# Optimization experiments

Measured on AMD Instinct MI355X. Metric: run time of the kernel, lower is better.

## Reference

```python
import jax, jax.numpy as jnp
import numpy as np

DIM = 768
HEADS = 12
HEAD_DIM = DIM // HEADS  # 64
GRID = 48               # H = W = 48 tokens
RANK = 8                # LoRA rank


def setup_inputs() -> dict:
    key = jax.random.key(0)
    ks = jax.random.split(key, 20)
    s = 0.02
    inp = {
        "x": jax.random.normal(ks[0], (1, GRID, GRID, DIM), dtype=jnp.float32),
        "Wq": jax.random.normal(ks[1], (DIM, DIM), dtype=jnp.float32) * s,
        "bq": jax.random.normal(ks[2], (DIM,), dtype=jnp.float32) * s,
        "Wk": jax.random.normal(ks[3], (DIM, DIM), dtype=jnp.float32) * s,
        "bk": jax.random.normal(ks[4], (DIM,), dtype=jnp.float32) * s,
        "Wv": jax.random.normal(ks[5], (DIM, DIM), dtype=jnp.float32) * s,
        "bv": jax.random.normal(ks[6], (DIM,), dtype=jnp.float32) * s,
        "Wp": jax.random.normal(ks[7], (DIM, DIM), dtype=jnp.float32) * s,
        "bp": jax.random.normal(ks[8], (DIM,), dtype=jnp.float32) * s,
        "rel_pos_h": jax.random.normal(ks[9], (2 * GRID - 1, HEAD_DIM), dtype=jnp.float32) * s,
        "rel_pos_w": jax.random.normal(ks[10], (2 * GRID - 1, HEAD_DIM), dtype=jnp.float32) * s,
        "Aq": jax.random.normal(ks[11], (DIM, RANK), dtype=jnp.float32) * s,
        "Bq": jax.random.normal(ks[12], (RANK, DIM), dtype=jnp.float32) * s,
        "Ak": jax.random.normal(ks[13], (DIM, RANK), dtype=jnp.float32) * s,
        "Bk": jax.random.normal(ks[14], (RANK, DIM), dtype=jnp.float32) * s,
        "Av": jax.random.normal(ks[15], (DIM, RANK), dtype=jnp.float32) * s,
        "Bv": jax.random.normal(ks[16], (RANK, DIM), dtype=jnp.float32) * s,
    }
    return inp


def _get_rel_pos(size, rel_pos):
    # q_size == k_size == size, rel_pos has exactly 2*size-1 rows -> direct lookup
    idx = jnp.arange(size)[:, None] - jnp.arange(size)[None, :] + (size - 1)
    return rel_pos[idx]  # (size, size, head_dim)


def reference(x, Wq, bq, Wk, bk, Wv, bv, Wp, bp, rel_pos_h, rel_pos_w,
              Aq, Bq, Ak, Bk, Av, Bv):
    B, H, W, _ = x.shape
    N = H * W
    scale = HEAD_DIM ** -0.5

    # QKV projections + LoRA additions
    q = x @ Wq + bq + (x @ Aq) @ Bq
    k = x @ Wk + bk + (x @ Ak) @ Bk
    v = x @ Wv + bv + (x @ Av) @ Bv

    # (B, heads, N, head_dim)
    q = q.reshape(B, N, HEADS, HEAD_DIM).transpose(0, 2, 1, 3)
    k = k.reshape(B, N, HEADS, HEAD_DIM).transpose(0, 2, 1, 3)
    v = v.reshape(B, N, HEADS, HEAD_DIM).transpose(0, 2, 1, 3)

    attn = jnp.einsum('bhnc,bhmc->bhnm', q, k) * scale  # (B, heads, N, N)

    # Decomposed relative position bias (SAM add_decomposed_rel_pos)
    Rh = _get_rel_pos(H, rel_pos_h)  # (H, H, c)
    Rw = _get_rel_pos(W, rel_pos_w)  # (W, W, c)
    r_q = q.reshape(B, HEADS, H, W, HEAD_DIM)
    rel_h = jnp.einsum('bnhwc,hkc->bnhwk', r_q, Rh)  # (B, heads, H, W, H)
    rel_w = jnp.einsum('bnhwc,wkc->bnhwk', r_q, Rw)  # (B, heads, H, W, W)
    attn = (attn.reshape(B, HEADS, H, W, H, W)
            + rel_h[..., :, None] + rel_w[..., None, :]).reshape(B, HEADS, N, N)

    attn = jax.nn.softmax(attn, axis=-1)
    out = jnp.einsum('bhnm,bhmc->bhnc', attn, v)        # (B, heads, N, c)
    out = out.transpose(0, 2, 1, 3).reshape(B, H, W, DIM)
    return out @ Wp + bp
```

## Files before the change

kernel.cpp:

```cpp
#include <hip/hip_runtime.h>


#define DIM   768
#define HEADS 12
#define HD    64
#define NTOK  2304
#define RANK  8
#define GRD   48
#define CHUNKS 4
#define LOG2E 1.44269504088896f

typedef __attribute__((ext_vector_type(8))) short bf16x8;
typedef __attribute__((ext_vector_type(4))) float f32x4;
typedef unsigned short ushort_t;

__device__ __forceinline__ unsigned short f2bf(float x) {
    union { float f; unsigned u; } v; v.f = x;
    unsigned r = v.u + 0x7fffu + ((v.u >> 16) & 1u);
    return (unsigned short)(r >> 16);
}
__device__ __forceinline__ float bf2f(unsigned short h) {
    return __uint_as_float(((unsigned)h) << 16);
}

__device__ __forceinline__ void gload_lds16(const ushort_t* g, ushort_t* l) {
    __builtin_amdgcn_global_load_lds(
        (const __attribute__((address_space(1))) unsigned int*)g,
        (__attribute__((address_space(3))) unsigned int*)l, 16, 0, 0);
}

__global__ __launch_bounds__(256) void k_convert_x(
    const float* __restrict__ x, ushort_t* __restrict__ xb,
    const float* __restrict__ rph, const float* __restrict__ rpw,
    ushort_t* __restrict__ rphb, ushort_t* __restrict__ rpwb) {
    if (blockIdx.x < 1728) {
        int idx = (blockIdx.x * 256 + threadIdx.x) * 4;
        float4 v = *(const float4*)(x + idx);
        ushort4 o = make_ushort4(f2bf(v.x), f2bf(v.y), f2bf(v.z), f2bf(v.w));
        *(ushort4*)(xb + idx) = o;
    } else {
        int e = ((blockIdx.x - 1728) * 256 + threadIdx.x) * 4;
        const int TSZ = (2 * GRD - 1) * HD;
        if (e < TSZ) {
            float4 v = *(const float4*)(rph + e);
            ushort4 o = make_ushort4(f2bf(v.x), f2bf(v.y), f2bf(v.z), f2bf(v.w));
            *(ushort4*)(rphb + e) = o;
        } else if (e < 2 * TSZ) {
            float4 v = *(const float4*)(rpw + e - TSZ);
            ushort4 o = make_ushort4(f2bf(v.x), f2bf(v.y), f2bf(v.z), f2bf(v.w));
            *(ushort4*)(rpwb + e - TSZ) = o;
        }
    }
}

__global__ __launch_bounds__(256) void k_fold(
    const float* __restrict__ Wq, const float* __restrict__ Wk,
    const float* __restrict__ Wv, const float* __restrict__ Wp,
    const float* __restrict__ Aq, const float* __restrict__ Bq,
    const float* __restrict__ Ak, const float* __restrict__ Bk,
    const float* __restrict__ Av, const float* __restrict__ Bv,
    ushort_t* __restrict__ WT) {
    int kb = blockIdx.x * 32;
    int nb = blockIdx.y * 32;
    int qkv = nb / DIM;
    int nmod = nb % DIM;
    const float* W = (qkv == 0) ? Wq : (qkv == 1) ? Wk : (qkv == 2) ? Wv : Wp;
    const float* A = (qkv == 0) ? Aq : (qkv == 1) ? Ak : Av;
    const float* B = (qkv == 0) ? Bq : (qkv == 1) ? Bk : Bv;

    __shared__ float T[32][33];
    for (int i = threadIdx.x; i < 1024; i += 256) {
        int kl = i / 32, nl = i % 32;
        float v = W[(kb + kl) * DIM + nmod + nl];
        if (qkv < 3) {
            #pragma unroll
            for (int r = 0; r < RANK; r++)
                v += A[(kb + kl) * RANK + r] * B[r * DIM + nmod + nl];
        }
        T[kl][nl] = v;
    }
    __syncthreads();
    for (int i = threadIdx.x; i < 1024; i += 256) {
        int nl = i / 32, kl = i % 32;
        WT[(size_t)(nb + nl) * DIM + kb + kl] = f2bf(T[kl][nl]);
    }
}

__global__ __launch_bounds__(256) void k_gemm_qkv(
    const ushort_t* __restrict__ xb, const ushort_t* __restrict__ WT,
    const float* __restrict__ bq, const float* __restrict__ bk,
    const float* __restrict__ bv,
    ushort_t* __restrict__ Qb, ushort_t* __restrict__ Kb,
    ushort_t* __restrict__ Vtb) {
    __shared__ __align__(16) ushort_t As[128 * 32];
    __shared__ __align__(16) ushort_t Bs[128 * 32];
    int tid = threadIdx.x;
    int wave = tid >> 6, lane = tid & 63, quad = lane >> 4, l16 = lane & 15;
    int wx = wave & 1, wy = wave >> 1;
    int nb = blockIdx.x * 128, mb = blockIdx.y * 128;

    f32x4 zero = {0.f, 0.f, 0.f, 0.f};
    f32x4 acc[4][4];
    #pragma unroll
    for (int i = 0; i < 4; i++)
        #pragma unroll
        for (int j = 0; j < 4; j++) acc[i][j] = zero;

    int rl = lane >> 2;
    int cl = (lane & 3) * 8;
    const ushort_t* gA = xb + (size_t)(mb + wave * 32 + rl) * DIM + cl;
    const ushort_t* gB = WT + (size_t)(nb + wave * 32 + rl) * DIM + cl;
    ushort_t* lA = &As[(wave * 32) * 32];
    ushort_t* lB = &Bs[(wave * 32) * 32];

    for (int k0 = 0; k0 < DIM; k0 += 32) {
        __syncthreads();
        gload_lds16(gA + k0,            lA);
        gload_lds16(gA + k0 + 16 * DIM, lA + 16 * 32);
        gload_lds16(gB + k0,            lB);
        gload_lds16(gB + k0 + 16 * DIM, lB + 16 * 32);
        __syncthreads();
        bf16x8 af[4], bf[4];
        #pragma unroll
        for (int i = 0; i < 4; i++)
            af[i] = *(const bf16x8*)&As[(wy * 64 + i * 16 + l16) * 32 + quad * 8];
        #pragma unroll
        for (int j = 0; j < 4; j++)
            bf[j] = *(const bf16x8*)&Bs[(wx * 64 + j * 16 + l16) * 32 + quad * 8];
        #pragma unroll
        for (int i = 0; i < 4; i++)
            #pragma unroll
            for (int j = 0; j < 4; j++)
                acc[i][j] = __builtin_amdgcn_mfma_f32_16x16x32_bf16(af[i], bf[j], acc[i][j], 0, 0, 0);
    }

    #pragma unroll
    for (int j = 0; j < 4; j++) {
        int col = nb + wx * 64 + j * 16 + l16;
        int qkv = col / DIM, rem = col % DIM;
        int hh = rem >> 6, cc = rem & 63;
        const float* bias = (qkv == 0) ? bq : (qkv == 1) ? bk : bv;
        float bval = bias[rem];
        #pragma unroll
        for (int i = 0; i < 4; i++) {
            #pragma unroll
            for (int r = 0; r < 4; r++) {
                int row = mb + wy * 64 + i * 16 + quad * 4 + r;
                unsigned short o = f2bf(acc[i][j][r] + bval);
                if (qkv == 0)      Qb[(size_t)(hh * NTOK + row) * HD + cc] = o;
                else if (qkv == 1) Kb[(size_t)(hh * NTOK + row) * HD + cc] = o;
                else               Vtb[(size_t)(hh * HD + cc) * NTOK + row] = o;
            }
        }
    }
}

__global__ __launch_bounds__(256) void k_relmm(
    const ushort_t* __restrict__ Qb, const ushort_t* __restrict__ rphb,
    const ushort_t* __restrict__ rpwb, float* __restrict__ relH,
    float* __restrict__ relW) {
    int id = blockIdx.x * 4 + (threadIdx.x >> 6);
    int lane = threadIdx.x & 63, quad = lane >> 4, l16 = lane & 15;
    bool isW = id >= 576;
    int t = isW ? id - 576 : id;
    int h = t / GRD, g = t % GRD;
    const ushort_t* tab = isW ? rpwb : rphb;
    float* outp = isW ? relW : relH;

    f32x4 zero = {0.f, 0.f, 0.f, 0.f};
    f32x4 acc[3][3];
    #pragma unroll
    for (int i = 0; i < 3; i++)
        #pragma unroll
        for (int j = 0; j < 3; j++) acc[i][j] = zero;

    bf16x8 bfr[3][2];
    #pragma unroll
    for (int ct = 0; ct < 3; ct++) {
        int trow = g + 47 - (ct * 16 + l16);
        bfr[ct][0] = *(const bf16x8*)&tab[(size_t)trow * HD + quad * 8];
        bfr[ct][1] = *(const bf16x8*)&tab[(size_t)trow * HD + 32 + quad * 8];
    }
    #pragma unroll
    for (int ms = 0; ms < 3; ms++) {
        int m = ms * 16 + l16;
        int n = isW ? m * GRD + g : g * GRD + m;
        bf16x8 a0 = *(const bf16x8*)&Qb[(size_t)(h * NTOK + n) * HD + quad * 8];
        bf16x8 a1 = *(const bf16x8*)&Qb[(size_t)(h * NTOK + n) * HD + 32 + quad * 8];
        #pragma unroll
        for (int ct = 0; ct < 3; ct++) {
            acc[ms][ct] = __builtin_amdgcn_mfma_f32_16x16x32_bf16(a0, bfr[ct][0], acc[ms][ct], 0, 0, 0);
            acc[ms][ct] = __builtin_amdgcn_mfma_f32_16x16x32_bf16(a1, bfr[ct][1], acc[ms][ct], 0, 0, 0);
        }
    }
    #pragma unroll
    for (int ms = 0; ms < 3; ms++) {
        #pragma unroll
        for (int ct = 0; ct < 3; ct++) {
            #pragma unroll
            for (int r = 0; r < 4; r++) {
                int m = ms * 16 + quad * 4 + r;
                int n = isW ? m * GRD + g : g * GRD + m;
                int col = ct * 16 + l16;
                outp[(size_t)(h * NTOK + n) * GRD + col] = acc[ms][ct][r] * LOG2E;
            }
        }
    }
}

__global__ __launch_bounds__(256) void k_attn(
    const ushort_t* __restrict__ Qb, const ushort_t* __restrict__ Kb,
    const ushort_t* __restrict__ Vtb, const float* __restrict__ relH,
    const float* __restrict__ relW, float* __restrict__ Opart,
    float* __restrict__ Lpart) {
    int h = blockIdx.x >> 2, chunk = blockIdx.x & 3, qt = blockIdx.y;
    int tid = threadIdx.x;
    int wave = tid >> 6, lane = tid & 63, quad = lane >> 4, l16 = lane & 15;
    int qbase = qt * 128;
    int kbase = chunk * 576;

    __shared__ __align__(16) ushort_t Ks[64 * 68];
    __shared__ __align__(16) ushort_t Vs[64 * 68];
    __shared__ __align__(16) ushort_t Ps[4][32 * 68];
    __shared__ __align__(16) ushort_t rws[128 * 52];
    __shared__ __align__(16) ushort_t rhs[128 * 14];

    for (int i = tid; i < 128 * 48; i += 256) {
        int r = i / 48, c = i % 48;
        rws[r * 52 + c] = f2bf(relW[(size_t)(h * NTOK + qbase + r) * GRD + c]);
    }
    for (int i = tid; i < 128 * 12; i += 256) {
        int r = i / 12, c = i % 12;
        rhs[r * 14 + c] = f2bf(relH[(size_t)(h * NTOK + qbase + r) * GRD + chunk * 12 + c]);
    }

    bf16x8 qf[2][2];
    #pragma unroll
    for (int s = 0; s < 2; s++) {
        int qrow = qbase + wave * 32 + s * 16 + l16;
        qf[s][0] = *(const bf16x8*)&Qb[(size_t)(h * NTOK + qrow) * HD + quad * 8];
        qf[s][1] = *(const bf16x8*)&Qb[(size_t)(h * NTOK + qrow) * HD + 32 + quad * 8];
    }

    int r0 = tid >> 3, c0 = (tid & 7) * 8;
    const ushort_t* kg0 = Kb + (size_t)(h * NTOK + r0) * HD + c0;
    const ushort_t* kg1 = Kb + (size_t)(h * NTOK + r0 + 32) * HD + c0;
    const ushort_t* vg0 = Vtb + (size_t)(h * HD + r0) * NTOK + c0;
    const ushort_t* vg1 = Vtb + (size_t)(h * HD + r0 + 32) * NTOK + c0;
    int sk0 = r0 * 68 + c0, sk1 = sk0 + 32 * 68;

    float lacc[2] = {0.f, 0.f};
    f32x4 zero = {0.f, 0.f, 0.f, 0.f};
    f32x4 oacc[2][4];
    #pragma unroll
    for (int s = 0; s < 2; s++)
        #pragma unroll
        for (int cs = 0; cs < 4; cs++) oacc[s][cs] = zero;

    const float scale2 = 0.125f * LOG2E;

    uint4 rk0 = *(const uint4*)(kg0 + (size_t)kbase * HD);
    uint4 rk1 = *(const uint4*)(kg1 + (size_t)kbase * HD);
    uint4 rv0 = *(const uint4*)(vg0 + kbase);
    uint4 rv1 = *(const uint4*)(vg1 + kbase);

    for (int kt = 0; kt < 9; kt++) {
        int kb = kbase + kt * 64;
        __syncthreads();
        *(uint4*)&Ks[sk0] = rk0;  *(uint4*)&Ks[sk1] = rk1;
        *(uint4*)&Vs[sk0] = rv0;  *(uint4*)&Vs[sk1] = rv1;
        __syncthreads();
        if (kt < 8) {
            int kbn = kb + 64;
            rk0 = *(const uint4*)(kg0 + (size_t)kbn * HD);
            rk1 = *(const uint4*)(kg1 + (size_t)kbn * HD);
            rv0 = *(const uint4*)(vg0 + kbn);
            rv1 = *(const uint4*)(vg1 + kbn);
        }

        #pragma unroll
        for (int ks = 0; ks < 4; ks++) {
            bf16x8 kf0 = *(const bf16x8*)&Ks[(ks * 16 + l16) * 68 + quad * 8];
            bf16x8 kf1 = *(const bf16x8*)&Ks[(ks * 16 + l16) * 68 + 32 + quad * 8];
            f32x4 st[2];
            #pragma unroll
            for (int s = 0; s < 2; s++) {
                f32x4 z = zero;
                z = __builtin_amdgcn_mfma_f32_16x16x32_bf16(kf0, qf[s][0], z, 0, 0, 0);
                z = __builtin_amdgcn_mfma_f32_16x16x32_bf16(kf1, qf[s][1], z, 0, 0, 0);
                st[s] = z;
            }
            int kb4 = kb + ks * 16 + quad * 4;
            int kh = kb4 / 48;
            int khl = kh - chunk * 12;
            int kw0 = kb4 - kh * 48;
            #pragma unroll
            for (int s = 0; s < 2; s++) {
                int row = wave * 32 + s * 16 + l16;
                float rh = bf2f(rhs[row * 14 + khl]);
                uint2 u = *(const uint2*)&rws[row * 52 + kw0];
                float p0 = __builtin_amdgcn_exp2f(st[s][0] * scale2 + rh + __uint_as_float(u.x << 16));
                float p1 = __builtin_amdgcn_exp2f(st[s][1] * scale2 + rh + __uint_as_float(u.x & 0xffff0000u));
                float p2 = __builtin_amdgcn_exp2f(st[s][2] * scale2 + rh + __uint_as_float(u.y << 16));
                float p3 = __builtin_amdgcn_exp2f(st[s][3] * scale2 + rh + __uint_as_float(u.y & 0xffff0000u));
                lacc[s] += (p0 + p1) + (p2 + p3);
                uint2 w;
                w.x = __builtin_amdgcn_perm(__float_as_uint(p1), __float_as_uint(p0), 0x07060302u);
                w.y = __builtin_amdgcn_perm(__float_as_uint(p3), __float_as_uint(p2), 0x07060302u);
                *(uint2*)&Ps[wave][(s * 16 + l16) * 68 + ks * 16 + quad * 4] = w;
            }
        }

        bf16x8 vf[4][2];
        #pragma unroll
        for (int cs = 0; cs < 4; cs++) {
            vf[cs][0] = *(const bf16x8*)&Vs[(cs * 16 + l16) * 68 + quad * 8];
            vf[cs][1] = *(const bf16x8*)&Vs[(cs * 16 + l16) * 68 + 32 + quad * 8];
        }
        #pragma unroll
        for (int s = 0; s < 2; s++) {
            bf16x8 pa0 = *(const bf16x8*)&Ps[wave][(s * 16 + l16) * 68 + quad * 8];
            bf16x8 pa1 = *(const bf16x8*)&Ps[wave][(s * 16 + l16) * 68 + 32 + quad * 8];
            #pragma unroll
            for (int cs = 0; cs < 4; cs++) {
                oacc[s][cs] = __builtin_amdgcn_mfma_f32_16x16x32_bf16(pa0, vf[cs][0], oacc[s][cs], 0, 0, 0);
                oacc[s][cs] = __builtin_amdgcn_mfma_f32_16x16x32_bf16(pa1, vf[cs][1], oacc[s][cs], 0, 0, 0);
            }
        }
    }

    #pragma unroll
    for (int s = 0; s < 2; s++) {
        float l = lacc[s];
        l += __shfl_xor(l, 16);
        l += __shfl_xor(l, 32);
        lacc[s] = l;
    }

    size_t obase = (size_t)(chunk * HEADS + h) * NTOK;
    #pragma unroll
    for (int s = 0; s < 2; s++) {
        #pragma unroll
        for (int cs = 0; cs < 4; cs++) {
            #pragma unroll
            for (int r = 0; r < 4; r++) {
                int row = qbase + wave * 32 + s * 16 + quad * 4 + r;
                Opart[(obase + row) * HD + cs * 16 + l16] = oacc[s][cs][r];
            }
        }
        if (quad == 0)
            Lpart[obase + qbase + wave * 32 + s * 16 + l16] = lacc[s];
    }
}

__global__ __launch_bounds__(256) void k_merge(const float* __restrict__ Opart,
                                               const float* __restrict__ Lpart,
                                               ushort_t* __restrict__ Ob) {
    int t = blockIdx.x * 256 + threadIdx.x;
    int e = t * 4;
    int c = e & (HD - 1);
    int row = (e >> 6) % NTOK;
    int h = e / (NTOK * HD);
    const int ostride = HEADS * NTOK * HD;
    float4 s = {0.f, 0.f, 0.f, 0.f};
    float l = 0.f;
    #pragma unroll
    for (int ch = 0; ch < CHUNKS; ch++) {
        float4 v = *(const float4*)&Opart[(size_t)ch * ostride + e];
        s.x += v.x; s.y += v.y; s.z += v.z; s.w += v.w;
        l += Lpart[(size_t)(ch * HEADS + h) * NTOK + row];
    }
    float inv = 1.0f / l;
    ushort4 o = make_ushort4(f2bf(s.x * inv), f2bf(s.y * inv),
                             f2bf(s.z * inv), f2bf(s.w * inv));
    *(ushort4*)&Ob[(size_t)row * DIM + h * HD + c] = o;
}

__global__ __launch_bounds__(256) void k_gemm_proj(
    const ushort_t* __restrict__ Ob, const ushort_t* __restrict__ WTp,
    const float* __restrict__ bp, float* __restrict__ out) {
    __shared__ __align__(16) ushort_t As[128 * 40];
    __shared__ __align__(16) ushort_t Bs[128 * 40];
    int tid = threadIdx.x;
    int wave = tid >> 6, lane = tid & 63, quad = lane >> 4, l16 = lane & 15;
    int wx = wave & 1, wy = wave >> 1;
    int nb = blockIdx.x * 128, mb = blockIdx.y * 128;

    f32x4 zero = {0.f, 0.f, 0.f, 0.f};
    f32x4 acc[4][4];
    #pragma unroll
    for (int i = 0; i < 4; i++)
        #pragma unroll
        for (int j = 0; j < 4; j++) acc[i][j] = zero;

    const ushort_t* Ag = Ob + (size_t)(mb + (tid >> 1)) * DIM + (tid & 1) * 16;
    const ushort_t* Bg = WTp + (size_t)(nb + (tid >> 1)) * DIM + (tid & 1) * 16;
    int sidx = (tid >> 1) * 40 + (tid & 1) * 16;

    for (int k0 = 0; k0 < DIM; k0 += 32) {
        uint4 a0 = *(const uint4*)(Ag + k0);
        uint4 a1 = *(const uint4*)(Ag + k0 + 8);
        uint4 b0 = *(const uint4*)(Bg + k0);
        uint4 b1 = *(const uint4*)(Bg + k0 + 8);
        __syncthreads();
        *(uint4*)&As[sidx] = a0;  *(uint4*)&As[sidx + 8] = a1;
        *(uint4*)&Bs[sidx] = b0;  *(uint4*)&Bs[sidx + 8] = b1;
        __syncthreads();
        bf16x8 af[4], bf[4];
        #pragma unroll
        for (int i = 0; i < 4; i++)
            af[i] = *(const bf16x8*)&As[(wy * 64 + i * 16 + l16) * 40 + quad * 8];
        #pragma unroll
        for (int j = 0; j < 4; j++)
            bf[j] = *(const bf16x8*)&Bs[(wx * 64 + j * 16 + l16) * 40 + quad * 8];
        #pragma unroll
        for (int i = 0; i < 4; i++)
            #pragma unroll
            for (int j = 0; j < 4; j++)
                acc[i][j] = __builtin_amdgcn_mfma_f32_16x16x32_bf16(af[i], bf[j], acc[i][j], 0, 0, 0);
    }

    #pragma unroll
    for (int j = 0; j < 4; j++) {
        int col = nb + wx * 64 + j * 16 + l16;
        float bval = bp[col];
        #pragma unroll
        for (int i = 0; i < 4; i++) {
            #pragma unroll
            for (int r = 0; r < 4; r++) {
                int row = mb + wy * 64 + i * 16 + quad * 4 + r;
                out[(size_t)row * DIM + col] = acc[i][j][r] + bval;
            }
        }
    }
}

extern "C" void kernel_launch(void* const* d_in, const int* in_sizes, int n_in,
                              void* d_out, int out_size, void* d_ws, size_t ws_size,
                              hipStream_t stream) {
    const float* x   = (const float*)d_in[0];
    const float* Wq  = (const float*)d_in[1];
    const float* bq  = (const float*)d_in[2];
    const float* Wk  = (const float*)d_in[3];
    const float* bk  = (const float*)d_in[4];
    const float* Wv  = (const float*)d_in[5];
    const float* bv  = (const float*)d_in[6];
    const float* Wp  = (const float*)d_in[7];
    const float* bp  = (const float*)d_in[8];
    const float* rph = (const float*)d_in[9];
    const float* rpw = (const float*)d_in[10];
    const float* Aq  = (const float*)d_in[11];
    const float* Bq  = (const float*)d_in[12];
    const float* Ak  = (const float*)d_in[13];
    const float* Bk  = (const float*)d_in[14];
    const float* Av  = (const float*)d_in[15];
    const float* Bv  = (const float*)d_in[16];
    float* out = (float*)d_out;

    char* w = (char*)d_ws;
    size_t off = 0;
    auto carve = [&](size_t bytes) {
        char* p = w + off;
        off += (bytes + 255) & ~(size_t)255;
        return p;
    };
    ushort_t* xb    = (ushort_t*)carve((size_t)NTOK * DIM * 2);
    ushort_t* WT    = (ushort_t*)carve((size_t)4 * DIM * DIM * 2);
    ushort_t* Qb    = (ushort_t*)carve((size_t)HEADS * NTOK * HD * 2);
    ushort_t* Kb    = (ushort_t*)carve((size_t)HEADS * NTOK * HD * 2);
    ushort_t* Vtb   = (ushort_t*)carve((size_t)HEADS * HD * NTOK * 2);
    float*    relH  = (float*)carve((size_t)HEADS * NTOK * GRD * 4);
    float*    relW  = (float*)carve((size_t)HEADS * NTOK * GRD * 4);
    ushort_t* Ob    = (ushort_t*)carve((size_t)NTOK * DIM * 2);
    float*    Opart = (float*)carve((size_t)CHUNKS * HEADS * NTOK * HD * 4);
    float*    Lpart = (float*)carve((size_t)CHUNKS * HEADS * NTOK * 4);
    ushort_t* rphb  = (ushort_t*)carve((size_t)(2 * GRD - 1) * HD * 2);
    ushort_t* rpwb  = (ushort_t*)carve((size_t)(2 * GRD - 1) * HD * 2);

    k_convert_x<<<dim3(1728 + 12), dim3(256), 0, stream>>>(x, xb, rph, rpw, rphb, rpwb);
    k_fold<<<dim3(DIM / 32, 4 * DIM / 32), dim3(256), 0, stream>>>(
        Wq, Wk, Wv, Wp, Aq, Bq, Ak, Bk, Av, Bv, WT);
    k_gemm_qkv<<<dim3(18, 18), dim3(256), 0, stream>>>(
        xb, WT, bq, bk, bv, Qb, Kb, Vtb);
    k_relmm<<<dim3(288), dim3(256), 0, stream>>>(
        Qb, rphb, rpwb, relH, relW);
    k_attn<<<dim3(HEADS * CHUNKS, NTOK / 128), dim3(256), 0, stream>>>(
        Qb, Kb, Vtb, relH, relW, Opart, Lpart);
    k_merge<<<dim3(HEADS * NTOK * HD / (256 * 4)), dim3(256), 0, stream>>>(
        Opart, Lpart, Ob);
    k_gemm_proj<<<dim3(6, 18), dim3(256), 0, stream>>>(
        Ob, WT + (size_t)3 * DIM * DIM, bp, out);
}
```

Baseline: 213.6 us.

## Fuse all stages into one cooperative persistent kernel with grid syncs

Replaces the seven separate launches with a single cooperative kernel of 768 persistent blocks. Each former kernel becomes a phase, and the phases are separated by grid-wide barriers. The attention phase also keeps the relW bias in registers as packed bf16 instead of staging it in shared memory, which cuts LDS use so four blocks fit per CU. This is meant to remove launch overhead and inter-kernel gaps, at the cost of grid-sync latency and of leaving many blocks idle in phases with few tiles (for example 108 blocks in the projection GEMM). A fallback to the multi-kernel path is kept for devices without cooperative launch support.

```diff
diff --git a/kernel.cpp b/kernel.cpp
--- a/kernel.cpp
+++ b/kernel.cpp
@@ -1,4 +1,7 @@
 #include <hip/hip_runtime.h>
+#include <hip/hip_cooperative_groups.h>
+
+namespace cg = cooperative_groups;
 
 
 #define DIM   768
@@ -9,6 +12,7 @@
 #define GRD   48
 #define CHUNKS 4
 #define LOG2E 1.44269504088896f
+#define NBLK  768
 
 typedef __attribute__((ext_vector_type(8))) short bf16x8;
 typedef __attribute__((ext_vector_type(4))) float f32x4;
@@ -22,11 +26,410 @@
 __device__ __forceinline__ float bf2f(unsigned short h) {
     return __uint_as_float(((unsigned)h) << 16);
 }
-
 __device__ __forceinline__ void gload_lds16(const ushort_t* g, ushort_t* l) {
     __builtin_amdgcn_global_load_lds(
         (const __attribute__((address_space(1))) unsigned int*)g,
         (__attribute__((address_space(3))) unsigned int*)l, 16, 0, 0);
+}
+
+struct MonoP {
+    const float *x, *Wq, *bq, *Wk, *bk, *Wv, *bv, *Wp, *bp, *rph, *rpw,
+                *Aq, *Bq, *Ak, *Bk, *Av, *Bv;
+    float *out;
+    ushort_t *xb, *WT, *Qb, *Kb, *Vtb, *Ob, *rphb, *rpwb;
+    float *relH, *relW, *Opart, *Lpart;
+};
+
+__global__ __launch_bounds__(256, 4) void k_mono(MonoP P) {
+    cg::grid_group gg = cg::this_grid();
+    __shared__ __align__(16) unsigned char smem[38912];
+    const int bid = blockIdx.x, tid = threadIdx.x;
+    const int wave = tid >> 6, lane = tid & 63, quad = lane >> 4, l16 = lane & 15;
+    const f32x4 zero = {0.f, 0.f, 0.f, 0.f};
+
+    for (int ct = bid; ct < 1740; ct += NBLK) {
+        if (ct < 1728) {
+            int idx = (ct * 256 + tid) * 4;
+            float4 v = *(const float4*)(P.x + idx);
+            ushort4 o = make_ushort4(f2bf(v.x), f2bf(v.y), f2bf(v.z), f2bf(v.w));
+            *(ushort4*)(P.xb + idx) = o;
+        } else {
+            int e = ((ct - 1728) * 256 + tid) * 4;
+            const int TSZ = (2 * GRD - 1) * HD;
+            if (e < TSZ) {
+                float4 v = *(const float4*)(P.rph + e);
+                ushort4 o = make_ushort4(f2bf(v.x), f2bf(v.y), f2bf(v.z), f2bf(v.w));
+                *(ushort4*)(P.rphb + e) = o;
+            } else if (e < 2 * TSZ) {
+                float4 v = *(const float4*)(P.rpw + e - TSZ);
+                ushort4 o = make_ushort4(f2bf(v.x), f2bf(v.y), f2bf(v.z), f2bf(v.w));
+                *(ushort4*)(P.rpwb + e - TSZ) = o;
+            }
+        }
+    }
+    {
+        float* T = (float*)smem;
+        for (int ft = bid; ft < 2304; ft += NBLK) {
+            int kb = (ft % 24) * 32, nb = (ft / 24) * 32;
+            int sel = nb / DIM, nmod = nb % DIM;
+            const float* W = (sel == 0) ? P.Wq : (sel == 1) ? P.Wk : (sel == 2) ? P.Wv : P.Wp;
+            const float* A = (sel == 0) ? P.Aq : (sel == 1) ? P.Ak : P.Av;
+            const float* B = (sel == 0) ? P.Bq : (sel == 1) ? P.Bk : P.Bv;
+            for (int i = tid; i < 1024; i += 256) {
+                int kl = i >> 5, nl = i & 31;
+                float v = W[(kb + kl) * DIM + nmod + nl];
+                if (sel < 3) {
+                    #pragma unroll
+                    for (int r = 0; r < RANK; r++)
+                        v += A[(kb + kl) * RANK + r] * B[r * DIM + nmod + nl];
+                }
+                T[kl * 33 + nl] = v;
+            }
+            __syncthreads();
+            for (int i = tid; i < 1024; i += 256) {
+                int nl = i >> 5, kl = i & 31;
+                P.WT[(size_t)(nb + nl) * DIM + kb + kl] = f2bf(T[kl * 33 + nl]);
+            }
+            __syncthreads();
+        }
+    }
+    gg.sync();
+
+    if (bid < 324) {
+        ushort_t* As = (ushort_t*)smem;
+        ushort_t* Bs = (ushort_t*)(smem + 8192);
+        int wx = wave & 1, wy = wave >> 1;
+        int nb = (bid % 18) * 128, mb = (bid / 18) * 128;
+
+        f32x4 acc[4][4];
+        #pragma unroll
+        for (int i = 0; i < 4; i++)
+            #pragma unroll
+            for (int j = 0; j < 4; j++) acc[i][j] = zero;
+
+        int rl = lane >> 2, cl = (lane & 3) * 8;
+        const ushort_t* gA = P.xb + (size_t)(mb + wave * 32 + rl) * DIM + cl;
+        const ushort_t* gB = P.WT + (size_t)(nb + wave * 32 + rl) * DIM + cl;
+        ushort_t* lA = &As[(wave * 32) * 32];
+        ushort_t* lB = &Bs[(wave * 32) * 32];
+
+        for (int k0 = 0; k0 < DIM; k0 += 32) {
+            __syncthreads();
+            gload_lds16(gA + k0,            lA);
+            gload_lds16(gA + k0 + 16 * DIM, lA + 16 * 32);
+            gload_lds16(gB + k0,            lB);
+            gload_lds16(gB + k0 + 16 * DIM, lB + 16 * 32);
+            __syncthreads();
+            bf16x8 af[4], bf[4];
+            #pragma unroll
+            for (int i = 0; i < 4; i++)
+                af[i] = *(const bf16x8*)&As[(wy * 64 + i * 16 + l16) * 32 + quad * 8];
+            #pragma unroll
+            for (int j = 0; j < 4; j++)
+                bf[j] = *(const bf16x8*)&Bs[(wx * 64 + j * 16 + l16) * 32 + quad * 8];
+            #pragma unroll
+            for (int i = 0; i < 4; i++)
+                #pragma unroll
+                for (int j = 0; j < 4; j++)
+                    acc[i][j] = __builtin_amdgcn_mfma_f32_16x16x32_bf16(af[i], bf[j], acc[i][j], 0, 0, 0);
+        }
+
+        #pragma unroll
+        for (int j = 0; j < 4; j++) {
+            int col = nb + wx * 64 + j * 16 + l16;
+            int sel = col / DIM, rem = col % DIM;
+            int hh = rem >> 6, cc = rem & 63;
+            const float* bias = (sel == 0) ? P.bq : (sel == 1) ? P.bk : P.bv;
+            float bval = bias[rem];
+            #pragma unroll
+            for (int i = 0; i < 4; i++) {
+                #pragma unroll
+                for (int r = 0; r < 4; r++) {
+                    int row = mb + wy * 64 + i * 16 + quad * 4 + r;
+                    unsigned short o = f2bf(acc[i][j][r] + bval);
+                    if (sel == 0)      P.Qb[(size_t)(hh * NTOK + row) * HD + cc] = o;
+                    else if (sel == 1) P.Kb[(size_t)(hh * NTOK + row) * HD + cc] = o;
+                    else               P.Vtb[(size_t)(hh * HD + cc) * NTOK + row] = o;
+                }
+            }
+        }
+    }
+    gg.sync();
+
+    if (bid < 288) {
+        int id = bid * 4 + wave;
+        bool isW = id >= 576;
+        int t = isW ? id - 576 : id;
+        int h = t / GRD, g = t % GRD;
+        const ushort_t* tab = isW ? P.rpwb : P.rphb;
+        float* outp = isW ? P.relW : P.relH;
+
+        f32x4 acc[3][3];
+        #pragma unroll
+        for (int i = 0; i < 3; i++)
+            #pragma unroll
+            for (int j = 0; j < 3; j++) acc[i][j] = zero;
+
+        bf16x8 bfr[3][2];
+        #pragma unroll
+        for (int ct = 0; ct < 3; ct++) {
+            int trow = g + 47 - (ct * 16 + l16);
+            bfr[ct][0] = *(const bf16x8*)&tab[(size_t)trow * HD + quad * 8];
+            bfr[ct][1] = *(const bf16x8*)&tab[(size_t)trow * HD + 32 + quad * 8];
+        }
+        #pragma unroll
+        for (int ms = 0; ms < 3; ms++) {
+            int m = ms * 16 + l16;
+            int n = isW ? m * GRD + g : g * GRD + m;
+            bf16x8 a0 = *(const bf16x8*)&P.Qb[(size_t)(h * NTOK + n) * HD + quad * 8];
+            bf16x8 a1 = *(const bf16x8*)&P.Qb[(size_t)(h * NTOK + n) * HD + 32 + quad * 8];
+            #pragma unroll
+            for (int ct = 0; ct < 3; ct++) {
+                acc[ms][ct] = __builtin_amdgcn_mfma_f32_16x16x32_bf16(a0, bfr[ct][0], acc[ms][ct], 0, 0, 0);
+                acc[ms][ct] = __builtin_amdgcn_mfma_f32_16x16x32_bf16(a1, bfr[ct][1], acc[ms][ct], 0, 0, 0);
+            }
+        }
+        #pragma unroll
+        for (int ms = 0; ms < 3; ms++) {
+            #pragma unroll
+            for (int ct = 0; ct < 3; ct++) {
+                #pragma unroll
+                for (int r = 0; r < 4; r++) {
+                    int m = ms * 16 + quad * 4 + r;
+                    int n = isW ? m * GRD + g : g * GRD + m;
+                    int col = ct * 16 + l16;
+                    outp[(size_t)(h * NTOK + n) * GRD + col] = acc[ms][ct][r] * LOG2E;
+                }
+            }
+        }
+    }
+    gg.sync();
+
+    for (int tile = bid; tile < 864; tile += NBLK) {
+        int xx = tile % 48, qt = tile / 48;
+        int h = xx >> 2, chunk = xx & 3;
+        int qbase = qt * 128, kbase = chunk * 576;
+
+        ushort_t* Ks  = (ushort_t*)smem;
+        ushort_t* Vs  = (ushort_t*)(smem + 8704);
+        ushort_t* Psw = (ushort_t*)(smem + 17408) + wave * (32 * 68);
+        ushort_t* rhs = (ushort_t*)(smem + 34816);
+
+        __syncthreads();
+
+        for (int i = tid; i < 128 * 12; i += 256) {
+            int r = i / 12, c = i % 12;
+            rhs[r * 14 + c] = f2bf(P.relH[(size_t)(h * NTOK + qbase + r) * GRD + chunk * 12 + c]);
+        }
+
+        bf16x8 qf[2][2];
+        #pragma unroll
+        for (int s = 0; s < 2; s++) {
+            int qrow = qbase + wave * 32 + s * 16 + l16;
+            qf[s][0] = *(const bf16x8*)&P.Qb[(size_t)(h * NTOK + qrow) * HD + quad * 8];
+            qf[s][1] = *(const bf16x8*)&P.Qb[(size_t)(h * NTOK + qrow) * HD + 32 + quad * 8];
+        }
+        uint2 rwreg[2][3];
+        #pragma unroll
+        for (int s = 0; s < 2; s++) {
+            int row = qbase + wave * 32 + s * 16 + l16;
+            const float* rp = P.relW + (size_t)(h * NTOK + row) * GRD + quad * 4;
+            #pragma unroll
+            for (int m3 = 0; m3 < 3; m3++) {
+                float4 rw = *(const float4*)(rp + m3 * 16);
+                uint2 u;
+                u.x = (unsigned)f2bf(rw.x) | ((unsigned)f2bf(rw.y) << 16);
+                u.y = (unsigned)f2bf(rw.z) | ((unsigned)f2bf(rw.w) << 16);
+                rwreg[s][m3] = u;
+            }
+        }
+
+        int r0 = tid >> 3, c0 = (tid & 7) * 8;
+        const ushort_t* kg0 = P.Kb + (size_t)(h * NTOK + r0) * HD + c0;
+        const ushort_t* kg1 = P.Kb + (size_t)(h * NTOK + r0 + 32) * HD + c0;
+        const ushort_t* vg0 = P.Vtb + (size_t)(h * HD + r0) * NTOK + c0;
+        const ushort_t* vg1 = P.Vtb + (size_t)(h * HD + r0 + 32) * NTOK + c0;
+        int sk0 = r0 * 68 + c0, sk1 = sk0 + 32 * 68;
+
+        float lacc[2] = {0.f, 0.f};
+        f32x4 oacc[2][4];
+        #pragma unroll
+        for (int s = 0; s < 2; s++)
+            #pragma unroll
+            for (int cs = 0; cs < 4; cs++) oacc[s][cs] = zero;
+
+        const float scale2 = 0.125f * LOG2E;
+
+        uint4 rk0 = *(const uint4*)(kg0 + (size_t)kbase * HD);
+        uint4 rk1 = *(const uint4*)(kg1 + (size_t)kbase * HD);
+        uint4 rv0 = *(const uint4*)(vg0 + kbase);
+        uint4 rv1 = *(const uint4*)(vg1 + kbase);
+
+        for (int kt = 0; kt < 9; kt++) {
+            int kb = kbase + kt * 64;
+            __syncthreads();
+            *(uint4*)&Ks[sk0] = rk0;  *(uint4*)&Ks[sk1] = rk1;
+            *(uint4*)&Vs[sk0] = rv0;  *(uint4*)&Vs[sk1] = rv1;
+            __syncthreads();
+            if (kt < 8) {
+                int kbn = kb + 64;
+                rk0 = *(const uint4*)(kg0 + (size_t)kbn * HD);
+                rk1 = *(const uint4*)(kg1 + (size_t)kbn * HD);
+                rv0 = *(const uint4*)(vg0 + kbn);
+                rv1 = *(const uint4*)(vg1 + kbn);
+            }
+
+            #pragma unroll
+            for (int ks = 0; ks < 4; ks++) {
+                bf16x8 kf0 = *(const bf16x8*)&Ks[(ks * 16 + l16) * 68 + quad * 8];
+                bf16x8 kf1 = *(const bf16x8*)&Ks[(ks * 16 + l16) * 68 + 32 + quad * 8];
+                f32x4 st[2];
+                #pragma unroll
+                for (int s = 0; s < 2; s++) {
+                    f32x4 z = zero;
+                    z = __builtin_amdgcn_mfma_f32_16x16x32_bf16(kf0, qf[s][0], z, 0, 0, 0);
+                    z = __builtin_amdgcn_mfma_f32_16x16x32_bf16(kf1, qf[s][1], z, 0, 0, 0);
+                    st[s] = z;
+                }
+                int kb4 = kb + ks * 16 + quad * 4;
+                int khl = kb4 / 48 - chunk * 12;
+                int m3 = (kt + ks) % 3;
+                #pragma unroll
+                for (int s = 0; s < 2; s++) {
+                    int row = wave * 32 + s * 16 + l16;
+                    float rh = bf2f(rhs[row * 14 + khl]);
+                    uint2 u = (m3 == 0) ? rwreg[s][0] : (m3 == 1) ? rwreg[s][1] : rwreg[s][2];
+                    float p0 = __builtin_amdgcn_exp2f(st[s][0] * scale2 + rh + __uint_as_float(u.x << 16));
+                    float p1 = __builtin_amdgcn_exp2f(st[s][1] * scale2 + rh + __uint_as_float(u.x & 0xffff0000u));
+                    float p2 = __builtin_amdgcn_exp2f(st[s][2] * scale2 + rh + __uint_as_float(u.y << 16));
+                    float p3 = __builtin_amdgcn_exp2f(st[s][3] * scale2 + rh + __uint_as_float(u.y & 0xffff0000u));
+                    lacc[s] += (p0 + p1) + (p2 + p3);
+                    uint2 w;
+                    w.x = __builtin_amdgcn_perm(__float_as_uint(p1), __float_as_uint(p0), 0x07060302u);
+                    w.y = __builtin_amdgcn_perm(__float_as_uint(p3), __float_as_uint(p2), 0x07060302u);
+                    *(uint2*)&Psw[(s * 16 + l16) * 68 + ks * 16 + quad * 4] = w;
+                }
+            }
+
+            bf16x8 vf[4][2];
+            #pragma unroll
+            for (int cs = 0; cs < 4; cs++) {
+                vf[cs][0] = *(const bf16x8*)&Vs[(cs * 16 + l16) * 68 + quad * 8];
+                vf[cs][1] = *(const bf16x8*)&Vs[(cs * 16 + l16) * 68 + 32 + quad * 8];
+            }
+            #pragma unroll
+            for (int s = 0; s < 2; s++) {
+                bf16x8 pa0 = *(const bf16x8*)&Psw[(s * 16 + l16) * 68 + quad * 8];
+                bf16x8 pa1 = *(const bf16x8*)&Psw[(s * 16 + l16) * 68 + 32 + quad * 8];
+                #pragma unroll
+                for (int cs = 0; cs < 4; cs++) {
+                    oacc[s][cs] = __builtin_amdgcn_mfma_f32_16x16x32_bf16(pa0, vf[cs][0], oacc[s][cs], 0, 0, 0);
+                    oacc[s][cs] = __builtin_amdgcn_mfma_f32_16x16x32_bf16(pa1, vf[cs][1], oacc[s][cs], 0, 0, 0);
+                }
+            }
+        }
+
+        #pragma unroll
+        for (int s = 0; s < 2; s++) {
+            float l = lacc[s];
+            l += __shfl_xor(l, 16);
+            l += __shfl_xor(l, 32);
+            lacc[s] = l;
+        }
+
+        size_t obase = (size_t)(chunk * HEADS + h) * NTOK;
+        #pragma unroll
+        for (int s = 0; s < 2; s++) {
+            #pragma unroll
+            for (int cs = 0; cs < 4; cs++) {
+                #pragma unroll
+                for (int r = 0; r < 4; r++) {
+                    int row = qbase + wave * 32 + s * 16 + quad * 4 + r;
+                    P.Opart[(obase + row) * HD + cs * 16 + l16] = oacc[s][cs][r];
+                }
+            }
+            if (quad == 0)
+                P.Lpart[obase + qbase + wave * 32 + s * 16 + l16] = lacc[s];
+        }
+    }
+    gg.sync();
+
+    for (int mt = bid; mt < 1728; mt += NBLK) {
+        int t = mt * 256 + tid;
+        int e = t * 4;
+        int c = e & (HD - 1);
+        int row = (e >> 6) % NTOK;
+        int h = e / (NTOK * HD);
+        const int ostride = HEADS * NTOK * HD;
+        float4 s4 = {0.f, 0.f, 0.f, 0.f};
+        float l = 0.f;
+        #pragma unroll
+        for (int ch = 0; ch < CHUNKS; ch++) {
+            float4 v = *(const float4*)&P.Opart[(size_t)ch * ostride + e];
+            s4.x += v.x; s4.y += v.y; s4.z += v.z; s4.w += v.w;
+            l += P.Lpart[(size_t)(ch * HEADS + h) * NTOK + row];
+        }
+        float inv = 1.0f / l;
+        ushort4 o = make_ushort4(f2bf(s4.x * inv), f2bf(s4.y * inv),
+                                 f2bf(s4.z * inv), f2bf(s4.w * inv));
+        *(ushort4*)&P.Ob[(size_t)row * DIM + h * HD + c] = o;
+    }
+    gg.sync();
+
+    if (bid < 108) {
+        ushort_t* As = (ushort_t*)smem;
+        ushort_t* Bs = (ushort_t*)(smem + 10240);
+        int wx = wave & 1, wy = wave >> 1;
+        int nb = (bid % 6) * 128, mb = (bid / 6) * 128;
+        const ushort_t* WTp = P.WT + (size_t)3 * DIM * DIM;
+
+        f32x4 acc[4][4];
+        #pragma unroll
+        for (int i = 0; i < 4; i++)
+            #pragma unroll
+            for (int j = 0; j < 4; j++) acc[i][j] = zero;
+
+        const ushort_t* Ag = P.Ob + (size_t)(mb + (tid >> 1)) * DIM + (tid & 1) * 16;
+        const ushort_t* Bg = WTp + (size_t)(nb + (tid >> 1)) * DIM + (tid & 1) * 16;
+        int sidx = (tid >> 1) * 40 + (tid & 1) * 16;
+
+        for (int k0 = 0; k0 < DIM; k0 += 32) {
+            uint4 a0 = *(const uint4*)(Ag + k0);
+            uint4 a1 = *(const uint4*)(Ag + k0 + 8);
+            uint4 b0 = *(const uint4*)(Bg + k0);
+            uint4 b1 = *(const uint4*)(Bg + k0 + 8);
+            __syncthreads();
+            *(uint4*)&As[sidx] = a0;  *(uint4*)&As[sidx + 8] = a1;
+            *(uint4*)&Bs[sidx] = b0;  *(uint4*)&Bs[sidx + 8] = b1;
+            __syncthreads();
+            bf16x8 af[4], bf[4];
+            #pragma unroll
+            for (int i = 0; i < 4; i++)
+                af[i] = *(const bf16x8*)&As[(wy * 64 + i * 16 + l16) * 40 + quad * 8];
+            #pragma unroll
+            for (int j = 0; j < 4; j++)
+                bf[j] = *(const bf16x8*)&Bs[(wx * 64 + j * 16 + l16) * 40 + quad * 8];
+            #pragma unroll
+            for (int i = 0; i < 4; i++)
+                #pragma unroll
+                for (int j = 0; j < 4; j++)
+                    acc[i][j] = __builtin_amdgcn_mfma_f32_16x16x32_bf16(af[i], bf[j], acc[i][j], 0, 0, 0);
+        }
+
+        #pragma unroll
+        for (int j = 0; j < 4; j++) {
+            int col = nb + wx * 64 + j * 16 + l16;
+            float bval = P.bp[col];
+            #pragma unroll
+            for (int i = 0; i < 4; i++) {
+                #pragma unroll
+                for (int r = 0; r < 4; r++) {
+                    int row = mb + wy * 64 + i * 16 + quad * 4 + r;
+                    P.out[(size_t)row * DIM + col] = acc[i][j][r] + bval;
+                }
+            }
+        }
+    }
 }
 
 __global__ __launch_bounds__(256) void k_convert_x(
@@ -62,17 +465,15 @@
     ushort_t* __restrict__ WT) {
     int kb = blockIdx.x * 32;
     int nb = blockIdx.y * 32;
-    int qkv = nb / DIM;
-    int nmod = nb % DIM;
-    const float* W = (qkv == 0) ? Wq : (qkv == 1) ? Wk : (qkv == 2) ? Wv : Wp;
-    const float* A = (qkv == 0) ? Aq : (qkv == 1) ? Ak : Av;
-    const float* B = (qkv == 0) ? Bq : (qkv == 1) ? Bk : Bv;
-
+    int sel = nb / DIM, nmod = nb % DIM;
+    const float* W = (sel == 0) ? Wq : (sel == 1) ? Wk : (sel == 2) ? Wv : Wp;
+    const float* A = (sel == 0) ? Aq : (sel == 1) ? Ak : Av;
+    const float* B = (sel == 0) ? Bq : (sel == 1) ? Bk : Bv;
     __shared__ float T[32][33];
     for (int i = threadIdx.x; i < 1024; i += 256) {
         int kl = i / 32, nl = i % 32;
         float v = W[(kb + kl) * DIM + nmod + nl];
-        if (qkv < 3) {
+        if (sel < 3) {
             #pragma unroll
             for (int r = 0; r < RANK; r++)
                 v += A[(kb + kl) * RANK + r] * B[r * DIM + nmod + nl];
@@ -98,21 +499,17 @@
     int wave = tid >> 6, lane = tid & 63, quad = lane >> 4, l16 = lane & 15;
     int wx = wave & 1, wy = wave >> 1;
     int nb = blockIdx.x * 128, mb = blockIdx.y * 128;
-
     f32x4 zero = {0.f, 0.f, 0.f, 0.f};
     f32x4 acc[4][4];
     #pragma unroll
     for (int i = 0; i < 4; i++)
         #pragma unroll
         for (int j = 0; j < 4; j++) acc[i][j] = zero;
-
-    int rl = lane >> 2;
-    int cl = (lane & 3) * 8;
+    int rl = lane >> 2, cl = (lane & 3) * 8;
     const ushort_t* gA = xb + (size_t)(mb + wave * 32 + rl) * DIM + cl;
     const ushort_t* gB = WT + (size_t)(nb + wave * 32 + rl) * DIM + cl;
     ushort_t* lA = &As[(wave * 32) * 32];
     ushort_t* lB = &Bs[(wave * 32) * 32];
-
     for (int k0 = 0; k0 < DIM; k0 += 32) {
         __syncthreads();
         gload_lds16(gA + k0,            lA);
@@ -133,13 +530,12 @@
             for (int j = 0; j < 4; j++)
                 acc[i][j] = __builtin_amdgcn_mfma_f32_16x16x32_bf16(af[i], bf[j], acc[i][j], 0, 0, 0);
     }
-
     #pragma unroll
     for (int j = 0; j < 4; j++) {
         int col = nb + wx * 64 + j * 16 + l16;
-        int qkv = col / DIM, rem = col % DIM;
+        int sel = col / DIM, rem = col % DIM;
         int hh = rem >> 6, cc = rem & 63;
-        const float* bias = (qkv == 0) ? bq : (qkv == 1) ? bk : bv;
+        const float* bias = (sel == 0) ? bq : (sel == 1) ? bk : bv;
         float bval = bias[rem];
         #pragma unroll
         for (int i = 0; i < 4; i++) {
@@ -147,8 +543,8 @@
             for (int r = 0; r < 4; r++) {
                 int row = mb + wy * 64 + i * 16 + quad * 4 + r;
                 unsigned short o = f2bf(acc[i][j][r] + bval);
-                if (qkv == 0)      Qb[(size_t)(hh * NTOK + row) * HD + cc] = o;
-                else if (qkv == 1) Kb[(size_t)(hh * NTOK + row) * HD + cc] = o;
+                if (sel == 0)      Qb[(size_t)(hh * NTOK + row) * HD + cc] = o;
+                else if (sel == 1) Kb[(size_t)(hh * NTOK + row) * HD + cc] = o;
                 else               Vtb[(size_t)(hh * HD + cc) * NTOK + row] = o;
             }
         }
@@ -166,14 +562,12 @@
     int h = t / GRD, g = t % GRD;
     const ushort_t* tab = isW ? rpwb : rphb;
     float* outp = isW ? relW : relH;
-
     f32x4 zero = {0.f, 0.f, 0.f, 0.f};
     f32x4 acc[3][3];
     #pragma unroll
     for (int i = 0; i < 3; i++)
         #pragma unroll
         for (int j = 0; j < 3; j++) acc[i][j] = zero;
-
     bf16x8 bfr[3][2];
     #pragma unroll
     for (int ct = 0; ct < 3; ct++) {
@@ -218,13 +612,11 @@
     int wave = tid >> 6, lane = tid & 63, quad = lane >> 4, l16 = lane & 15;
     int qbase = qt * 128;
     int kbase = chunk * 576;
-
     __shared__ __align__(16) ushort_t Ks[64 * 68];
     __shared__ __align__(16) ushort_t Vs[64 * 68];
     __shared__ __align__(16) ushort_t Ps[4][32 * 68];
     __shared__ __align__(16) ushort_t rws[128 * 52];
     __shared__ __align__(16) ushort_t rhs[128 * 14];
-
     for (int i = tid; i < 128 * 48; i += 256) {
         int r = i / 48, c = i % 48;
         rws[r * 52 + c] = f2bf(relW[(size_t)(h * NTOK + qbase + r) * GRD + c]);
@@ -233,7 +625,6 @@
         int r = i / 12, c = i % 12;
         rhs[r * 14 + c] = f2bf(relH[(size_t)(h * NTOK + qbase + r) * GRD + chunk * 12 + c]);
     }
-
     bf16x8 qf[2][2];
     #pragma unroll
     for (int s = 0; s < 2; s++) {
@@ -241,14 +632,12 @@
         qf[s][0] = *(const bf16x8*)&Qb[(size_t)(h * NTOK + qrow) * HD + quad * 8];
         qf[s][1] = *(const bf16x8*)&Qb[(size_t)(h * NTOK + qrow) * HD + 32 + quad * 8];
     }
-
     int r0 = tid >> 3, c0 = (tid & 7) * 8;
     const ushort_t* kg0 = Kb + (size_t)(h * NTOK + r0) * HD + c0;
     const ushort_t* kg1 = Kb + (size_t)(h * NTOK + r0 + 32) * HD + c0;
     const ushort_t* vg0 = Vtb + (size_t)(h * HD + r0) * NTOK + c0;
     const ushort_t* vg1 = Vtb + (size_t)(h * HD + r0 + 32) * NTOK + c0;
     int sk0 = r0 * 68 + c0, sk1 = sk0 + 32 * 68;
-
     float lacc[2] = {0.f, 0.f};
     f32x4 zero = {0.f, 0.f, 0.f, 0.f};
     f32x4 oacc[2][4];
@@ -256,14 +645,11 @@
     for (int s = 0; s < 2; s++)
         #pragma unroll
         for (int cs = 0; cs < 4; cs++) oacc[s][cs] = zero;
-
     const float scale2 = 0.125f * LOG2E;
-
     uint4 rk0 = *(const uint4*)(kg0 + (size_t)kbase * HD);
     uint4 rk1 = *(const uint4*)(kg1 + (size_t)kbase * HD);
     uint4 rv0 = *(const uint4*)(vg0 + kbase);
     uint4 rv1 = *(const uint4*)(vg1 + kbase);
-
     for (int kt = 0; kt < 9; kt++) {
         int kb = kbase + kt * 64;
         __syncthreads();
@@ -277,7 +663,6 @@
             rv0 = *(const uint4*)(vg0 + kbn);
             rv1 = *(const uint4*)(vg1 + kbn);
         }
-
         #pragma unroll
         for (int ks = 0; ks < 4; ks++) {
             bf16x8 kf0 = *(const bf16x8*)&Ks[(ks * 16 + l16) * 68 + quad * 8];
@@ -310,7 +695,6 @@
                 *(uint2*)&Ps[wave][(s * 16 + l16) * 68 + ks * 16 + quad * 4] = w;
             }
         }
-
         bf16x8 vf[4][2];
         #pragma unroll
         for (int cs = 0; cs < 4; cs++) {
@@ -328,7 +712,6 @@
             }
         }
     }
-
     #pragma unroll
     for (int s = 0; s < 2; s++) {
         float l = lacc[s];
@@ -336,7 +719,6 @@
         l += __shfl_xor(l, 32);
         lacc[s] = l;
     }
-
     size_t obase = (size_t)(chunk * HEADS + h) * NTOK;
     #pragma unroll
     for (int s = 0; s < 2; s++) {
@@ -385,18 +767,15 @@
     int wave = tid >> 6, lane = tid & 63, quad = lane >> 4, l16 = lane & 15;
     int wx = wave & 1, wy = wave >> 1;
     int nb = blockIdx.x * 128, mb = blockIdx.y * 128;
-
     f32x4 zero = {0.f, 0.f, 0.f, 0.f};
     f32x4 acc[4][4];
     #pragma unroll
     for (int i = 0; i < 4; i++)
         #pragma unroll
         for (int j = 0; j < 4; j++) acc[i][j] = zero;
-
     const ushort_t* Ag = Ob + (size_t)(mb + (tid >> 1)) * DIM + (tid & 1) * 16;
     const ushort_t* Bg = WTp + (size_t)(nb + (tid >> 1)) * DIM + (tid & 1) * 16;
     int sidx = (tid >> 1) * 40 + (tid & 1) * 16;
-
     for (int k0 = 0; k0 < DIM; k0 += 32) {
         uint4 a0 = *(const uint4*)(Ag + k0);
         uint4 a1 = *(const uint4*)(Ag + k0 + 8);
@@ -419,7 +798,6 @@
             for (int j = 0; j < 4; j++)
                 acc[i][j] = __builtin_amdgcn_mfma_f32_16x16x32_bf16(af[i], bf[j], acc[i][j], 0, 0, 0);
     }
-
     #pragma unroll
     for (int j = 0; j < 4; j++) {
         int col = nb + wx * 64 + j * 16 + l16;
@@ -477,17 +855,36 @@
     ushort_t* rphb  = (ushort_t*)carve((size_t)(2 * GRD - 1) * HD * 2);
     ushort_t* rpwb  = (ushort_t*)carve((size_t)(2 * GRD - 1) * HD * 2);
 
-    k_convert_x<<<dim3(1728 + 12), dim3(256), 0, stream>>>(x, xb, rph, rpw, rphb, rpwb);
-    k_fold<<<dim3(DIM / 32, 4 * DIM / 32), dim3(256), 0, stream>>>(
-        Wq, Wk, Wv, Wp, Aq, Bq, Ak, Bk, Av, Bv, WT);
-    k_gemm_qkv<<<dim3(18, 18), dim3(256), 0, stream>>>(
-        xb, WT, bq, bk, bv, Qb, Kb, Vtb);
-    k_relmm<<<dim3(288), dim3(256), 0, stream>>>(
-        Qb, rphb, rpwb, relH, relW);
-    k_attn<<<dim3(HEADS * CHUNKS, NTOK / 128), dim3(256), 0, stream>>>(
-        Qb, Kb, Vtb, relH, relW, Opart, Lpart);
-    k_merge<<<dim3(HEADS * NTOK * HD / (256 * 4)), dim3(256), 0, stream>>>(
-        Opart, Lpart, Ob);
-    k_gemm_proj<<<dim3(6, 18), dim3(256), 0, stream>>>(
-        Ob, WT + (size_t)3 * DIM * DIM, bp, out);
-}
+    int coop = 0, dev = 0, maxblk = 0;
+    hipGetDevice(&dev);
+    hipDeviceGetAttribute(&coop, hipDeviceAttributeCooperativeLaunch, dev);
+    hipOccupancyMaxActiveBlocksPerMultiprocessor(&maxblk, (const void*)k_mono, 256, 0);
+
+    if (coop && maxblk >= 3) {
+        MonoP P;
+        P.x = x; P.Wq = Wq; P.bq = bq; P.Wk = Wk; P.bk = bk; P.Wv = Wv; P.bv = bv;
+        P.Wp = Wp; P.bp = bp; P.rph = rph; P.rpw = rpw;
+        P.Aq = Aq; P.Bq = Bq; P.Ak = Ak; P.Bk = Bk; P.Av = Av; P.Bv = Bv;
+        P.out = out;
+        P.xb = xb; P.WT = WT; P.Qb = Qb; P.Kb = Kb; P.Vtb = Vtb; P.Ob = Ob;
+        P.rphb = rphb; P.rpwb = rpwb;
+        P.relH = relH; P.relW = relW; P.Opart = Opart; P.Lpart = Lpart;
+        void* args[] = { (void*)&P };
+        hipLaunchCooperativeKernel((const void*)k_mono, dim3(NBLK), dim3(256),
+                                   args, 0, stream);
+    } else {
+        k_convert_x<<<dim3(1728 + 12), dim3(256), 0, stream>>>(x, xb, rph, rpw, rphb, rpwb);
+        k_fold<<<dim3(DIM / 32, 4 * DIM / 32), dim3(256), 0, stream>>>(
+            Wq, Wk, Wv, Wp, Aq, Bq, Ak, Bk, Av, Bv, WT);
+        k_gemm_qkv<<<dim3(18, 18), dim3(256), 0, stream>>>(
+            xb, WT, bq, bk, bv, Qb, Kb, Vtb);
+        k_relmm<<<dim3(288), dim3(256), 0, stream>>>(
+            Qb, rphb, rpwb, relH, relW);
+        k_attn<<<dim3(HEADS * CHUNKS, NTOK / 128), dim3(256), 0, stream>>>(
+            Qb, Kb, Vtb, relH, relW, Opart, Lpart);
+        k_merge<<<dim3(HEADS * NTOK * HD / (256 * 4)), dim3(256), 0, stream>>>(
+            Opart, Lpart, Ob);
+        k_gemm_proj<<<dim3(6, 18), dim3(256), 0, stream>>>(
+            Ob, WT + (size_t)3 * DIM * DIM, bp, out);
+    }
+}
```

Result: no change. 216.3 us (+1.3%).
